# Kernel optimization log

Measured on AMD Instinct MI355X. Metric: run time of the kernel, lower is better.

## Reference

```python
import jax, jax.numpy as jnp
import numpy as np

LATENT, HID = 32, 64
NODE_FEAT, EDGE_FEAT, ENERGY_DIM, STRESS_DIM = 4, 3, 2, 9
B, N, E = 256, 200000, 1500000


def _lin(key, fan_in, fan_out):
    kw, kb = jax.random.split(key)
    s = 1.0 / np.sqrt(fan_in)
    return (jax.random.uniform(kw, (fan_in, fan_out), jnp.float32, -s, s),
            jax.random.uniform(kb, (fan_out,), jnp.float32, -s, s))


def setup_inputs() -> dict:
    key = jax.random.key(0)
    ks = jax.random.split(key, 16)
    z = jax.random.normal(ks[0], (B, LATENT), jnp.float32)
    node_emb = jax.random.normal(ks[1], (N, 2 * HID), jnp.float32)
    graph_id = jnp.sort(jax.random.randint(ks[2], (N,), 0, B))
    src = jax.random.randint(ks[3], (E,), 0, N)
    dst = jax.random.randint(ks[4], (E,), 0, N)
    lp_w, lp_b = _lin(ks[5], LATENT, 2 * HID)            # latent_proj
    nep_w, nep_b = _lin(ks[6], 2 * HID, 2 * HID)          # node_emb_proj
    nd1_w, nd1_b = _lin(ks[7], 2 * HID, HID)              # node_decoder L1
    nd2_w, nd2_b = _lin(ks[8], HID, NODE_FEAT)            # node_decoder L2
    ed1_w, ed1_b = _lin(ks[9], 4 * HID, HID)              # edge_decoder L1
    ed2_w, ed2_b = _lin(ks[10], HID, EDGE_FEAT)           # edge_decoder L2
    en1_w, en1_b = _lin(ks[11], LATENT, HID)              # energy L1
    en2_w, en2_b = _lin(ks[12], HID, ENERGY_DIM)          # energy L2
    st1_w, st1_b = _lin(ks[13], LATENT, HID)              # stress L1
    st2_w, st2_b = _lin(ks[14], HID, STRESS_DIM)          # stress L2
    return dict(z=z, node_emb=node_emb, graph_id=graph_id, src=src, dst=dst,
                lp_w=lp_w, lp_b=lp_b, nep_w=nep_w, nep_b=nep_b,
                nd1_w=nd1_w, nd1_b=nd1_b, nd2_w=nd2_w, nd2_b=nd2_b,
                ed1_w=ed1_w, ed1_b=ed1_b, ed2_w=ed2_w, ed2_b=ed2_b,
                en1_w=en1_w, en1_b=en1_b, en2_w=en2_w, en2_b=en2_b,
                st1_w=st1_w, st1_b=st1_b, st2_w=st2_w, st2_b=st2_b)


def reference(z, node_emb, graph_id, src, dst,
              lp_w, lp_b, nep_w, nep_b, nd1_w, nd1_b, nd2_w, nd2_b,
              ed1_w, ed1_b, ed2_w, ed2_b, en1_w, en1_b, en2_w, en2_b,
              st1_w, st1_b, st2_w, st2_b):
    # latent_proj + per-graph broadcast (gather replaces the Python loop)
    z_proj = jax.nn.relu(z @ lp_w + lp_b)            # [B, 2H]
    z_expanded = z_proj[graph_id]                    # [N, 2H]
    # node reconstruction (dropout is identity in eval)
    nep = jax.nn.relu(node_emb @ nep_w + nep_b)      # [N, 2H]
    h = z_expanded + nep
    recon_node = jax.nn.relu(h @ nd1_w + nd1_b) @ nd2_w + nd2_b    # [N, 4]
    # edge reconstruction: gather-concat + small MLP
    edge_input = jnp.concatenate([z_expanded[src], z_expanded[dst]], axis=1)  # [E, 4H]
    recon_edge = jax.nn.relu(edge_input @ ed1_w + ed1_b) @ ed2_w + ed2_b       # [E, 3]
    # graph-level predictors
    pred_energy = jax.nn.relu(z @ en1_w + en1_b) @ en2_w + en2_b   # [B, 2]
    pred_stress = jax.nn.relu(z @ st1_w + st1_b) @ st2_w + st2_b   # [B, 9]
    return recon_node, recon_edge, pred_energy, pred_stress
```

## Files before the change

### kernel.cpp

```cpp
#include <hip/hip_runtime.h>
#include <hip/hip_bf16.h>

#define LATENT 32
#define HID 64
#define NB 256
#define NN 200000
#define NE 1500000
#define TWOH 128

#define OUT_NODE_OFF   0
#define OUT_EDGE_OFF   (NN * 4)
#define OUT_ENERGY_OFF (OUT_EDGE_OFF + NE * 3)
#define OUT_STRESS_OFF (OUT_ENERGY_OFF + NB * 2)

#define WS_ZPROJ 0
#define WS_ZC    (WS_ZPROJ + NB*TWOH)
#define WS_P1    (WS_ZC + NB*HID)
#define WS_P2    (WS_P1 + NB*HID)
#define WS_T4    (WS_P2 + NB*HID)
#define WS_W1T   (WS_T4 + NB*NB*4)
#define WS_W2T   (WS_W1T + 8192)

typedef _Float16 half8 __attribute__((ext_vector_type(8)));
typedef _Float16 half4 __attribute__((ext_vector_type(4)));
typedef float f32x4 __attribute__((ext_vector_type(4)));

__global__ void precompute_kernel(
    const float* __restrict__ z,
    const float* __restrict__ lp_w, const float* __restrict__ lp_b,
    const float* __restrict__ nd1_w,
    const float* __restrict__ ed1_w,
    const float* __restrict__ en1_w, const float* __restrict__ en1_b,
    const float* __restrict__ en2_w, const float* __restrict__ en2_b,
    const float* __restrict__ st1_w, const float* __restrict__ st1_b,
    const float* __restrict__ st2_w, const float* __restrict__ st2_b,
    float* __restrict__ z_proj, float* __restrict__ zc,
    float* __restrict__ P1, float* __restrict__ P2,
    float* __restrict__ out_energy, float* __restrict__ out_stress)
{
    const int b = blockIdx.x;
    const int t = threadIdx.x;

    __shared__ float zrow[LATENT];
    __shared__ float zp[TWOH];
    __shared__ float h_en[HID];
    __shared__ float h_st[HID];

    if (t < LATENT) zrow[t] = z[b * LATENT + t];
    __syncthreads();

    {
        float a = lp_b[t];
        #pragma unroll
        for (int k = 0; k < LATENT; ++k)
            a = fmaf(zrow[k], lp_w[k * TWOH + t], a);
        a = fmaxf(a, 0.f);
        zp[t] = a;
        z_proj[b * TWOH + t] = a;
    }

    if (t < HID) {
        float ae = en1_b[t];
        float as = st1_b[t];
        #pragma unroll
        for (int k = 0; k < LATENT; ++k) {
            ae = fmaf(zrow[k], en1_w[k * HID + t], ae);
            as = fmaf(zrow[k], st1_w[k * HID + t], as);
        }
        h_en[t] = fmaxf(ae, 0.f);
        h_st[t] = fmaxf(as, 0.f);
    }
    __syncthreads();

    if (t < HID) {
        float a = 0.f, p1 = 0.f, p2 = 0.f;
        #pragma unroll 8
        for (int k = 0; k < TWOH; ++k) {
            const float zk = zp[k];
            a  = fmaf(zk, nd1_w[k * HID + t], a);
            p1 = fmaf(zk, ed1_w[k * HID + t], p1);
            p2 = fmaf(zk, ed1_w[(TWOH + k) * HID + t], p2);
        }
        zc[b * HID + t] = a;
        P1[b * HID + t] = p1;
        P2[b * HID + t] = p2;
    }

    if (t < 2) {
        float a = en2_b[t];
        #pragma unroll 8
        for (int k = 0; k < HID; ++k) a = fmaf(h_en[k], en2_w[k * 2 + t], a);
        out_energy[b * 2 + t] = a;
    }
    if (t >= 16 && t < 25) {
        const int j = t - 16;
        float a = st2_b[j];
        #pragma unroll 8
        for (int k = 0; k < HID; ++k) a = fmaf(h_st[k], st2_w[k * 9 + j], a);
        out_stress[b * 9 + j] = a;
    }
}

__global__ void prep_weights_kernel(
    const float* __restrict__ nep_w, const float* __restrict__ nd1_w,
    _Float16* __restrict__ w1T, _Float16* __restrict__ w2T)
{
    const int i = blockIdx.x * 256 + threadIdx.x;
    if (i < TWOH * TWOH) {
        const int n = i >> 7, k = i & 127;
        w1T[i] = (_Float16)nep_w[k * TWOH + n];
    }
    if (i < HID * TWOH) {
        const int n = i >> 7, k = i & 127;
        w2T[i] = (_Float16)nd1_w[k * HID + n];
    }
}

__global__ void edge_table_kernel(
    const float* __restrict__ P1, const float* __restrict__ P2,
    const float* __restrict__ ed1_b,
    const float* __restrict__ ed2_w, const float* __restrict__ ed2_b,
    float4* __restrict__ T4)
{
    const int gs = blockIdx.x;
    const int t  = threadIdx.x;

    __shared__ float p1s[HID];
    __shared__ float b1s[HID];
    __shared__ float w2s[HID * 3];
    __shared__ float b2s[3];

    if (t < HID) { p1s[t] = P1[gs * HID + t]; b1s[t] = ed1_b[t]; }
    if (t >= 64 && t < 64 + HID * 3) w2s[t - 64] = ed2_w[t - 64];
    if (t < 3) b2s[t] = ed2_b[t];
    __syncthreads();

    float o0 = b2s[0], o1 = b2s[1], o2 = b2s[2];
    const float* __restrict__ p2 = &P2[t * HID];
    #pragma unroll 8
    for (int k = 0; k < HID; ++k) {
        float h = fmaxf(p1s[k] + p2[k] + b1s[k], 0.f);
        o0 = fmaf(h, w2s[k * 3 + 0], o0);
        o1 = fmaf(h, w2s[k * 3 + 1], o1);
        o2 = fmaf(h, w2s[k * 3 + 2], o2);
    }
    T4[gs * NB + t] = make_float4(o0, o1, o2, 0.f);
}

#define MT 64
#define SWZ(r) (((r) & 15) << 3)

__global__ __launch_bounds__(256, 2)
void node_kernel(
    const float* __restrict__ node_emb,
    const int*   __restrict__ graph_id,
    const _Float16* __restrict__ w1T,
    const float* __restrict__ nep_b,
    const _Float16* __restrict__ w2T,
    const float* __restrict__ nd1_b,
    const float* __restrict__ nd2_w, const float* __restrict__ nd2_b,
    const float* __restrict__ zc,
    float* __restrict__ out_node)
{
    __shared__ _Float16 embT[MT * TWOH];
    __shared__ _Float16 nep [MT * TWOH];
    __shared__ float    tt  [MT * 69];
    __shared__ float    w3  [HID * 4];
    __shared__ int      gid_s[MT];

    const int tid = threadIdx.x;
    const int n0  = blockIdx.x * MT;

    {
        const int c4 = tid & 31;
        #pragma unroll
        for (int pass = 0; pass < 8; ++pass) {
            const int row = (tid >> 5) + pass * 8;
            const float4 v = *reinterpret_cast<const float4*>(
                node_emb + (size_t)(n0 + row) * TWOH + c4 * 4);
            half4 h;
            h[0] = (_Float16)v.x; h[1] = (_Float16)v.y;
            h[2] = (_Float16)v.z; h[3] = (_Float16)v.w;
            const int e = row * TWOH + c4 * 4;
            *reinterpret_cast<half4*>(&embT[e ^ SWZ(row)]) = h;
        }
        if (tid < MT) gid_s[tid] = graph_id[n0 + tid];
        w3[tid] = nd2_w[tid];
    }
    __syncthreads();

    const int wv   = tid >> 6;
    const int lane = tid & 63;
    const int lrow = lane & 15;
    const int kg   = lane >> 4;

    {
        half8 a[4];
        #pragma unroll
        for (int kb = 0; kb < 4; ++kb) {
            const int r = wv * 16 + lrow;
            const int e = r * TWOH + kb * 32 + kg * 8;
            a[kb] = *reinterpret_cast<const half8*>(&embT[e ^ SWZ(r)]);
        }
        f32x4 acc[8];
        #pragma unroll
        for (int tn = 0; tn < 8; ++tn) acc[tn] = (f32x4){0.f, 0.f, 0.f, 0.f};

        #pragma unroll
        for (int tn = 0; tn < 8; ++tn) {
            const int n = tn * 16 + lrow;
            #pragma unroll
            for (int kb = 0; kb < 4; ++kb) {
                const half8 b = *reinterpret_cast<const half8*>(
                    &w1T[n * TWOH + kb * 32 + kg * 8]);
                acc[tn] = __builtin_amdgcn_mfma_f32_16x16x32_f16(a[kb], b, acc[tn], 0, 0, 0);
            }
        }
        #pragma unroll
        for (int tn = 0; tn < 8; ++tn) {
            const int n = tn * 16 + lrow;
            const float bn = nep_b[n];
            #pragma unroll
            for (int reg = 0; reg < 4; ++reg) {
                const int r = wv * 16 + kg * 4 + reg;
                const float v = fmaxf(acc[tn][reg] + bn, 0.f);
                nep[(r * TWOH + n) ^ SWZ(r)] = (_Float16)v;
            }
        }
    }
    __syncthreads();

    {
        half8 a2[4];
        #pragma unroll
        for (int kb = 0; kb < 4; ++kb) {
            const int r = wv * 16 + lrow;
            const int e = r * TWOH + kb * 32 + kg * 8;
            a2[kb] = *reinterpret_cast<const half8*>(&nep[e ^ SWZ(r)]);
        }
        f32x4 acc2[4];
        #pragma unroll
        for (int tn = 0; tn < 4; ++tn) acc2[tn] = (f32x4){0.f, 0.f, 0.f, 0.f};

        #pragma unroll
        for (int tn = 0; tn < 4; ++tn) {
            const int n = tn * 16 + lrow;
            #pragma unroll
            for (int kb = 0; kb < 4; ++kb) {
                const half8 b = *reinterpret_cast<const half8*>(
                    &w2T[n * TWOH + kb * 32 + kg * 8]);
                acc2[tn] = __builtin_amdgcn_mfma_f32_16x16x32_f16(a2[kb], b, acc2[tn], 0, 0, 0);
            }
        }
        #pragma unroll
        for (int tn = 0; tn < 4; ++tn) {
            const int n = tn * 16 + lrow;
            const float b1 = nd1_b[n];
            #pragma unroll
            for (int reg = 0; reg < 4; ++reg) {
                const int r = wv * 16 + kg * 4 + reg;
                const int g = gid_s[r];
                const float v = fmaxf(acc2[tn][reg] + b1 + zc[g * HID + n], 0.f);
                tt[r * 69 + n] = v;
            }
        }
    }
    __syncthreads();

    {
        const int nd = tid >> 2;
        const int o  = tid & 3;
        float a = nd2_b[o];
        #pragma unroll 8
        for (int k = 0; k < HID; ++k)
            a = fmaf(tt[nd * 69 + k], w3[k * 4 + o], a);
        out_node[(size_t)(n0 + nd) * 4 + o] = a;
    }
}

__global__ void edge_kernel(
    const int* __restrict__ src, const int* __restrict__ dst,
    const int* __restrict__ graph_id,
    const float4* __restrict__ T4,
    float* __restrict__ out_edge)
{
    const int e0 = (blockIdx.x * 256 + threadIdx.x) * 4;
    if (e0 >= NE) return;
    const int4 s4 = *reinterpret_cast<const int4*>(&src[e0]);
    const int4 d4 = *reinterpret_cast<const int4*>(&dst[e0]);
    const int ss[4] = {s4.x, s4.y, s4.z, s4.w};
    const int dd[4] = {d4.x, d4.y, d4.z, d4.w};
    float o[12];
    #pragma unroll
    for (int j = 0; j < 4; ++j) {
        const int gs = graph_id[ss[j]];
        const int gd = graph_id[dd[j]];
        const float4 t = T4[gs * NB + gd];
        o[j * 3 + 0] = t.x; o[j * 3 + 1] = t.y; o[j * 3 + 2] = t.z;
    }
    float4* outp = reinterpret_cast<float4*>(&out_edge[(size_t)e0 * 3]);
    outp[0] = make_float4(o[0], o[1], o[2],  o[3]);
    outp[1] = make_float4(o[4], o[5], o[6],  o[7]);
    outp[2] = make_float4(o[8], o[9], o[10], o[11]);
}

extern "C" void kernel_launch(void* const* d_in, const int* in_sizes, int n_in,
                              void* d_out, int out_size, void* d_ws, size_t ws_size,
                              hipStream_t stream)
{
    const float* z        = (const float*)d_in[0];
    const float* node_emb = (const float*)d_in[1];
    const int*   graph_id = (const int*)  d_in[2];
    const int*   src      = (const int*)  d_in[3];
    const int*   dst      = (const int*)  d_in[4];
    const float* lp_w  = (const float*)d_in[5];
    const float* lp_b  = (const float*)d_in[6];
    const float* nep_w = (const float*)d_in[7];
    const float* nep_b = (const float*)d_in[8];
    const float* nd1_w = (const float*)d_in[9];
    const float* nd1_b = (const float*)d_in[10];
    const float* nd2_w = (const float*)d_in[11];
    const float* nd2_b = (const float*)d_in[12];
    const float* ed1_w = (const float*)d_in[13];
    const float* ed1_b = (const float*)d_in[14];
    const float* ed2_w = (const float*)d_in[15];
    const float* ed2_b = (const float*)d_in[16];
    const float* en1_w = (const float*)d_in[17];
    const float* en1_b = (const float*)d_in[18];
    const float* en2_w = (const float*)d_in[19];
    const float* en2_b = (const float*)d_in[20];
    const float* st1_w = (const float*)d_in[21];
    const float* st1_b = (const float*)d_in[22];
    const float* st2_w = (const float*)d_in[23];
    const float* st2_b = (const float*)d_in[24];

    float* out = (float*)d_out;
    float* out_node   = out + OUT_NODE_OFF;
    float* out_edge   = out + OUT_EDGE_OFF;
    float* out_energy = out + OUT_ENERGY_OFF;
    float* out_stress = out + OUT_STRESS_OFF;

    float* ws     = (float*)d_ws;
    float* z_proj = ws + WS_ZPROJ;
    float* zc     = ws + WS_ZC;
    float* P1     = ws + WS_P1;
    float* P2     = ws + WS_P2;
    float4* T4    = (float4*)(ws + WS_T4);
    _Float16* w1T = (_Float16*)(ws + WS_W1T);
    _Float16* w2T = (_Float16*)(ws + WS_W2T);

    precompute_kernel<<<NB, 128, 0, stream>>>(
        z, lp_w, lp_b, nd1_w, ed1_w,
        en1_w, en1_b, en2_w, en2_b, st1_w, st1_b, st2_w, st2_b,
        z_proj, zc, P1, P2, out_energy, out_stress);

    prep_weights_kernel<<<64, 256, 0, stream>>>(nep_w, nd1_w, w1T, w2T);

    edge_table_kernel<<<NB, NB, 0, stream>>>(P1, P2, ed1_b, ed2_w, ed2_b, T4);

    node_kernel<<<NN / MT, 256, 0, stream>>>(
        node_emb, graph_id, w1T, nep_b, w2T, nd1_b, nd2_w, nd2_b,
        zc, out_node);

    edge_kernel<<<(NE / 4 + 255) / 256, 256, 0, stream>>>(
        src, dst, graph_id, T4, out_edge);
}
```

Before: 310.6 us.

## Fuse node and edge kernels into persistent pipelined kernel with register-resident weights

Merges the node MLP and edge gather kernels into one launch. Node blocks become persistent (512 blocks looping over tiles) and double-buffer the node_emb tile, prefetching the next tile into registers while MFMAs run on the current one. Weights are held in registers as the A operand instead of being reloaded from global memory for every tile. The final layer becomes a register dot product plus cross-lane shuffle reduction instead of a shared-memory loop. Weight prep is also folded into the precompute launch to save a kernel launch. The cost is higher register pressure and fewer node blocks, which may limit occupancy or parallelism.

```diff
diff --git a/kernel.cpp b/kernel.cpp
--- a/kernel.cpp
+++ b/kernel.cpp
@@ -24,6 +24,12 @@
 typedef _Float16 half8 __attribute__((ext_vector_type(8)));
 typedef _Float16 half4 __attribute__((ext_vector_type(4)));
 typedef float f32x4 __attribute__((ext_vector_type(4)));
+
+#define MT 64
+#define NTILES (NN / MT)
+#define NODE_BLOCKS 512
+#define EDGE_BLOCKS ((NE / 4 + 255) / 256)
+#define SWZ(r) (((r) & 15) << 3)
 
 __global__ void precompute_kernel(
     const float* __restrict__ z,
@@ -34,13 +40,28 @@
     const float* __restrict__ en2_w, const float* __restrict__ en2_b,
     const float* __restrict__ st1_w, const float* __restrict__ st1_b,
     const float* __restrict__ st2_w, const float* __restrict__ st2_b,
+    const float* __restrict__ nep_w,
     float* __restrict__ z_proj, float* __restrict__ zc,
     float* __restrict__ P1, float* __restrict__ P2,
+    _Float16* __restrict__ w1T, _Float16* __restrict__ w2T,
     float* __restrict__ out_energy, float* __restrict__ out_stress)
 {
+    const int t = threadIdx.x;
+
+    if (blockIdx.x >= NB) {
+        const int i = (blockIdx.x - NB) * 256 + t;
+        if (i < TWOH * TWOH) {
+            const int n = i >> 7, k = i & 127;
+            w1T[i] = (_Float16)nep_w[k * TWOH + n];
+        }
+        if (i < HID * TWOH) {
+            const int n = i >> 7, k = i & 127;
+            w2T[i] = (_Float16)nd1_w[k * HID + n];
+        }
+        return;
+    }
+
     const int b = blockIdx.x;
-    const int t = threadIdx.x;
-
     __shared__ float zrow[LATENT];
     __shared__ float zp[TWOH];
     __shared__ float h_en[HID];
@@ -49,7 +70,7 @@
     if (t < LATENT) zrow[t] = z[b * LATENT + t];
     __syncthreads();
 
-    {
+    if (t < TWOH) {
         float a = lp_b[t];
         #pragma unroll
         for (int k = 0; k < LATENT; ++k)
@@ -58,7 +79,6 @@
         zp[t] = a;
         z_proj[b * TWOH + t] = a;
     }
-
     if (t < HID) {
         float ae = en1_b[t];
         float as = st1_b[t];
@@ -85,7 +105,6 @@
         P1[b * HID + t] = p1;
         P2[b * HID + t] = p2;
     }
-
     if (t < 2) {
         float a = en2_b[t];
         #pragma unroll 8
@@ -98,21 +117,6 @@
         #pragma unroll 8
         for (int k = 0; k < HID; ++k) a = fmaf(h_st[k], st2_w[k * 9 + j], a);
         out_stress[b * 9 + j] = a;
-    }
-}
-
-__global__ void prep_weights_kernel(
-    const float* __restrict__ nep_w, const float* __restrict__ nd1_w,
-    _Float16* __restrict__ w1T, _Float16* __restrict__ w2T)
-{
-    const int i = blockIdx.x * 256 + threadIdx.x;
-    if (i < TWOH * TWOH) {
-        const int n = i >> 7, k = i & 127;
-        w1T[i] = (_Float16)nep_w[k * TWOH + n];
-    }
-    if (i < HID * TWOH) {
-        const int n = i >> 7, k = i & 127;
-        w2T[i] = (_Float16)nd1_w[k * HID + n];
     }
 }
 
@@ -147,11 +151,8 @@
     T4[gs * NB + t] = make_float4(o0, o1, o2, 0.f);
 }
 
-#define MT 64
-#define SWZ(r) (((r) & 15) << 3)
-
 __global__ __launch_bounds__(256, 2)
-void node_kernel(
+void node_edge_kernel(
     const float* __restrict__ node_emb,
     const int*   __restrict__ graph_id,
     const _Float16* __restrict__ w1T,
@@ -160,148 +161,219 @@
     const float* __restrict__ nd1_b,
     const float* __restrict__ nd2_w, const float* __restrict__ nd2_b,
     const float* __restrict__ zc,
-    float* __restrict__ out_node)
+    const int* __restrict__ src, const int* __restrict__ dst,
+    const float4* __restrict__ T4,
+    float* __restrict__ out_node, float* __restrict__ out_edge)
 {
-    __shared__ _Float16 embT[MT * TWOH];
-    __shared__ _Float16 nep [MT * TWOH];
-    __shared__ float    tt  [MT * 69];
-    __shared__ float    w3  [HID * 4];
-    __shared__ int      gid_s[MT];
-
     const int tid = threadIdx.x;
-    const int n0  = blockIdx.x * MT;
-
-    {
-        const int c4 = tid & 31;
-        #pragma unroll
-        for (int pass = 0; pass < 8; ++pass) {
-            const int row = (tid >> 5) + pass * 8;
-            const float4 v = *reinterpret_cast<const float4*>(
-                node_emb + (size_t)(n0 + row) * TWOH + c4 * 4);
-            half4 h;
-            h[0] = (_Float16)v.x; h[1] = (_Float16)v.y;
-            h[2] = (_Float16)v.z; h[3] = (_Float16)v.w;
-            const int e = row * TWOH + c4 * 4;
-            *reinterpret_cast<half4*>(&embT[e ^ SWZ(row)]) = h;
-        }
-        if (tid < MT) gid_s[tid] = graph_id[n0 + tid];
-        w3[tid] = nd2_w[tid];
-    }
-    __syncthreads();
+    const int bid = blockIdx.x;
+
+    if (bid >= NODE_BLOCKS) {
+        const int e0 = ((bid - NODE_BLOCKS) * 256 + tid) * 4;
+        if (e0 >= NE) return;
+        const int4 s4 = *reinterpret_cast<const int4*>(&src[e0]);
+        const int4 d4 = *reinterpret_cast<const int4*>(&dst[e0]);
+        const int ss[4] = {s4.x, s4.y, s4.z, s4.w};
+        const int dd[4] = {d4.x, d4.y, d4.z, d4.w};
+        float o[12];
+        #pragma unroll
+        for (int j = 0; j < 4; ++j) {
+            const int gs = graph_id[ss[j]];
+            const int gd = graph_id[dd[j]];
+            const float4 tv = T4[gs * NB + gd];
+            o[j * 3 + 0] = tv.x; o[j * 3 + 1] = tv.y; o[j * 3 + 2] = tv.z;
+        }
+        float4* outp = reinterpret_cast<float4*>(&out_edge[(size_t)e0 * 3]);
+        outp[0] = make_float4(o[0], o[1], o[2],  o[3]);
+        outp[1] = make_float4(o[4], o[5], o[6],  o[7]);
+        outp[2] = make_float4(o[8], o[9], o[10], o[11]);
+        return;
+    }
+
+    __shared__ _Float16 embL[2][MT * TWOH];
+    __shared__ _Float16 nepL[MT * TWOH];
+    __shared__ float    partL[4 * MT * 4];
+    __shared__ int      gidL[2][MT];
 
     const int wv   = tid >> 6;
     const int lane = tid & 63;
     const int lrow = lane & 15;
     const int kg   = lane >> 4;
 
+    half8 w1A[2][4];
+    half8 w2A[4];
+    #pragma unroll
+    for (int cht = 0; cht < 2; ++cht)
+        #pragma unroll
+        for (int kb = 0; kb < 4; ++kb)
+            w1A[cht][kb] = *reinterpret_cast<const half8*>(
+                &w1T[(wv * 32 + cht * 16 + lrow) * TWOH + kb * 32 + kg * 8]);
+    #pragma unroll
+    for (int kb = 0; kb < 4; ++kb)
+        w2A[kb] = *reinterpret_cast<const half8*>(
+            &w2T[(wv * 16 + lrow) * TWOH + kb * 32 + kg * 8]);
+
+    f32x4 b1r[2], b2r, w3r[4];
+    #pragma unroll
+    for (int cht = 0; cht < 2; ++cht)
+        b1r[cht] = *reinterpret_cast<const f32x4*>(&nep_b[wv * 32 + cht * 16 + kg * 4]);
+    b2r = *reinterpret_cast<const f32x4*>(&nd1_b[wv * 16 + kg * 4]);
+    #pragma unroll
+    for (int j = 0; j < 4; ++j)
+        w3r[j] = *reinterpret_cast<const f32x4*>(&nd2_w[(wv * 16 + kg * 4 + j) * 4]);
+    const float b3 = nd2_b[tid & 3];
+
+    const int r0 = tid >> 2;
+    const int q0 = tid & 3;
+
     {
-        half8 a[4];
-        #pragma unroll
-        for (int kb = 0; kb < 4; ++kb) {
-            const int r = wv * 16 + lrow;
-            const int e = r * TWOH + kb * 32 + kg * 8;
-            a[kb] = *reinterpret_cast<const half8*>(&embT[e ^ SWZ(r)]);
-        }
-        f32x4 acc[8];
-        #pragma unroll
-        for (int tn = 0; tn < 8; ++tn) acc[tn] = (f32x4){0.f, 0.f, 0.f, 0.f};
-
-        #pragma unroll
-        for (int tn = 0; tn < 8; ++tn) {
-            const int n = tn * 16 + lrow;
+        const float4* s4 = reinterpret_cast<const float4*>(
+            node_emb + (size_t)(bid * MT + r0) * TWOH);
+        float4 rr[8];
+        #pragma unroll
+        for (int p = 0; p < 8; ++p) rr[p] = s4[q0 + 4 * p];
+        #pragma unroll
+        for (int p = 0; p < 8; ++p) {
+            half4 h;
+            h[0] = (_Float16)rr[p].x; h[1] = (_Float16)rr[p].y;
+            h[2] = (_Float16)rr[p].z; h[3] = (_Float16)rr[p].w;
+            const int e = r0 * TWOH + (q0 + 4 * p) * 4;
+            *reinterpret_cast<half4*>(&embL[0][e ^ SWZ(r0)]) = h;
+        }
+        if (tid < MT) gidL[0][tid] = graph_id[bid * MT + tid];
+    }
+    __syncthreads();
+
+    int cur = 0;
+    for (int t = bid; t < NTILES; t += NODE_BLOCKS) {
+        const int tn = t + NODE_BLOCKS;
+        const bool have_next = (tn < NTILES);
+
+        float4 rr[8];
+        int gnext = 0;
+        if (have_next) {
+            const float4* s4 = reinterpret_cast<const float4*>(
+                node_emb + (size_t)(tn * MT + r0) * TWOH);
+            #pragma unroll
+            for (int p = 0; p < 8; ++p) rr[p] = s4[q0 + 4 * p];
+            if (tid < MT) gnext = graph_id[tn * MT + tid];
+        }
+
+        const _Float16* eb = embL[cur];
+
+        f32x4 acc1[2][4];
+        #pragma unroll
+        for (int cht = 0; cht < 2; ++cht)
+            #pragma unroll
+            for (int nt = 0; nt < 4; ++nt)
+                acc1[cht][nt] = (f32x4){0.f, 0.f, 0.f, 0.f};
+
+        #pragma unroll
+        for (int nt = 0; nt < 4; ++nt) {
+            half8 eB[4];
             #pragma unroll
             for (int kb = 0; kb < 4; ++kb) {
-                const half8 b = *reinterpret_cast<const half8*>(
-                    &w1T[n * TWOH + kb * 32 + kg * 8]);
-                acc[tn] = __builtin_amdgcn_mfma_f32_16x16x32_f16(a[kb], b, acc[tn], 0, 0, 0);
+                const int row = nt * 16 + lrow;
+                const int e = row * TWOH + kb * 32 + kg * 8;
+                eB[kb] = *reinterpret_cast<const half8*>(&eb[e ^ SWZ(row)]);
             }
-        }
-        #pragma unroll
-        for (int tn = 0; tn < 8; ++tn) {
-            const int n = tn * 16 + lrow;
-            const float bn = nep_b[n];
-            #pragma unroll
-            for (int reg = 0; reg < 4; ++reg) {
-                const int r = wv * 16 + kg * 4 + reg;
-                const float v = fmaxf(acc[tn][reg] + bn, 0.f);
-                nep[(r * TWOH + n) ^ SWZ(r)] = (_Float16)v;
+            #pragma unroll
+            for (int cht = 0; cht < 2; ++cht)
+                #pragma unroll
+                for (int kb = 0; kb < 4; ++kb)
+                    acc1[cht][nt] = __builtin_amdgcn_mfma_f32_16x16x32_f16(
+                        w1A[cht][kb], eB[kb], acc1[cht][nt], 0, 0, 0);
+        }
+        #pragma unroll
+        for (int cht = 0; cht < 2; ++cht)
+            #pragma unroll
+            for (int nt = 0; nt < 4; ++nt) {
+                const int node = nt * 16 + lrow;
+                const int ch = wv * 32 + cht * 16 + kg * 4;
+                half4 h;
+                #pragma unroll
+                for (int j = 0; j < 4; ++j)
+                    h[j] = (_Float16)fmaxf(acc1[cht][nt][j] + b1r[cht][j], 0.f);
+                *reinterpret_cast<half4*>(
+                    &nepL[(node * TWOH + ch) ^ SWZ(node)]) = h;
             }
-        }
-    }
-    __syncthreads();
-
-    {
-        half8 a2[4];
-        #pragma unroll
-        for (int kb = 0; kb < 4; ++kb) {
-            const int r = wv * 16 + lrow;
-            const int e = r * TWOH + kb * 32 + kg * 8;
-            a2[kb] = *reinterpret_cast<const half8*>(&nep[e ^ SWZ(r)]);
-        }
+        __syncthreads();
+
         f32x4 acc2[4];
         #pragma unroll
-        for (int tn = 0; tn < 4; ++tn) acc2[tn] = (f32x4){0.f, 0.f, 0.f, 0.f};
-
-        #pragma unroll
-        for (int tn = 0; tn < 4; ++tn) {
-            const int n = tn * 16 + lrow;
+        for (int nt = 0; nt < 4; ++nt) acc2[nt] = (f32x4){0.f, 0.f, 0.f, 0.f};
+
+        #pragma unroll
+        for (int nt = 0; nt < 4; ++nt) {
+            half8 nB[4];
             #pragma unroll
             for (int kb = 0; kb < 4; ++kb) {
-                const half8 b = *reinterpret_cast<const half8*>(
-                    &w2T[n * TWOH + kb * 32 + kg * 8]);
-                acc2[tn] = __builtin_amdgcn_mfma_f32_16x16x32_f16(a2[kb], b, acc2[tn], 0, 0, 0);
+                const int row = nt * 16 + lrow;
+                const int e = row * TWOH + kb * 32 + kg * 8;
+                nB[kb] = *reinterpret_cast<const half8*>(&nepL[e ^ SWZ(row)]);
             }
-        }
-        #pragma unroll
-        for (int tn = 0; tn < 4; ++tn) {
-            const int n = tn * 16 + lrow;
-            const float b1 = nd1_b[n];
-            #pragma unroll
-            for (int reg = 0; reg < 4; ++reg) {
-                const int r = wv * 16 + kg * 4 + reg;
-                const int g = gid_s[r];
-                const float v = fmaxf(acc2[tn][reg] + b1 + zc[g * HID + n], 0.f);
-                tt[r * 69 + n] = v;
+            #pragma unroll
+            for (int kb = 0; kb < 4; ++kb)
+                acc2[nt] = __builtin_amdgcn_mfma_f32_16x16x32_f16(
+                    w2A[kb], nB[kb], acc2[nt], 0, 0, 0);
+        }
+
+        f32x4 p[4];
+        #pragma unroll
+        for (int nt = 0; nt < 4; ++nt) {
+            const int node = nt * 16 + lrow;
+            const int g = gidL[cur][node];
+            const f32x4 z4 = *reinterpret_cast<const f32x4*>(
+                &zc[(size_t)g * HID + wv * 16 + kg * 4]);
+            f32x4 t4;
+            #pragma unroll
+            for (int j = 0; j < 4; ++j)
+                t4[j] = fmaxf(acc2[nt][j] + b2r[j] + z4[j], 0.f);
+            f32x4 pp = t4[0] * w3r[0];
+            pp += t4[1] * w3r[1];
+            pp += t4[2] * w3r[2];
+            pp += t4[3] * w3r[3];
+            p[nt] = pp;
+        }
+        #pragma unroll
+        for (int nt = 0; nt < 4; ++nt) {
+            #pragma unroll
+            for (int j = 0; j < 4; ++j) {
+                p[nt][j] += __shfl_xor(p[nt][j], 16, 64);
+                p[nt][j] += __shfl_xor(p[nt][j], 32, 64);
             }
         }
-    }
-    __syncthreads();
-
-    {
-        const int nd = tid >> 2;
-        const int o  = tid & 3;
-        float a = nd2_b[o];
-        #pragma unroll 8
-        for (int k = 0; k < HID; ++k)
-            a = fmaf(tt[nd * 69 + k], w3[k * 4 + o], a);
-        out_node[(size_t)(n0 + nd) * 4 + o] = a;
-    }
-}
-
-__global__ void edge_kernel(
-    const int* __restrict__ src, const int* __restrict__ dst,
-    const int* __restrict__ graph_id,
-    const float4* __restrict__ T4,
-    float* __restrict__ out_edge)
-{
-    const int e0 = (blockIdx.x * 256 + threadIdx.x) * 4;
-    if (e0 >= NE) return;
-    const int4 s4 = *reinterpret_cast<const int4*>(&src[e0]);
-    const int4 d4 = *reinterpret_cast<const int4*>(&dst[e0]);
-    const int ss[4] = {s4.x, s4.y, s4.z, s4.w};
-    const int dd[4] = {d4.x, d4.y, d4.z, d4.w};
-    float o[12];
-    #pragma unroll
-    for (int j = 0; j < 4; ++j) {
-        const int gs = graph_id[ss[j]];
-        const int gd = graph_id[dd[j]];
-        const float4 t = T4[gs * NB + gd];
-        o[j * 3 + 0] = t.x; o[j * 3 + 1] = t.y; o[j * 3 + 2] = t.z;
-    }
-    float4* outp = reinterpret_cast<float4*>(&out_edge[(size_t)e0 * 3]);
-    outp[0] = make_float4(o[0], o[1], o[2],  o[3]);
-    outp[1] = make_float4(o[4], o[5], o[6],  o[7]);
-    outp[2] = make_float4(o[8], o[9], o[10], o[11]);
+        if (lane < 16) {
+            #pragma unroll
+            for (int nt = 0; nt < 4; ++nt)
+                *reinterpret_cast<f32x4*>(
+                    &partL[(wv * MT + nt * 16 + lrow) * 4]) = p[nt];
+        }
+        __syncthreads();
+
+        {
+            const int node = r0;
+            const int o    = q0;
+            const int ix = node * 4 + o;
+            const float s = partL[ix] + partL[256 + ix] +
+                            partL[512 + ix] + partL[768 + ix] + b3;
+            out_node[(size_t)(t * MT + node) * 4 + o] = s;
+        }
+
+        if (have_next) {
+            #pragma unroll
+            for (int p8 = 0; p8 < 8; ++p8) {
+                half4 h;
+                h[0] = (_Float16)rr[p8].x; h[1] = (_Float16)rr[p8].y;
+                h[2] = (_Float16)rr[p8].z; h[3] = (_Float16)rr[p8].w;
+                const int e = r0 * TWOH + (q0 + 4 * p8) * 4;
+                *reinterpret_cast<half4*>(&embL[cur ^ 1][e ^ SWZ(r0)]) = h;
+            }
+            if (tid < MT) gidL[cur ^ 1][tid] = gnext;
+        }
+        __syncthreads();
+        cur ^= 1;
+    }
 }
 
 extern "C" void kernel_launch(void* const* d_in, const int* in_sizes, int n_in,
@@ -349,19 +421,14 @@
     _Float16* w1T = (_Float16*)(ws + WS_W1T);
     _Float16* w2T = (_Float16*)(ws + WS_W2T);
 
-    precompute_kernel<<<NB, 128, 0, stream>>>(
+    precompute_kernel<<<NB + 64, 256, 0, stream>>>(
         z, lp_w, lp_b, nd1_w, ed1_w,
-        en1_w, en1_b, en2_w, en2_b, st1_w, st1_b, st2_w, st2_b,
-        z_proj, zc, P1, P2, out_energy, out_stress);
-
-    prep_weights_kernel<<<64, 256, 0, stream>>>(nep_w, nd1_w, w1T, w2T);
+        en1_w, en1_b, en2_w, en2_b, st1_w, st1_b, st2_w, st2_b, nep_w,
+        z_proj, zc, P1, P2, w1T, w2T, out_energy, out_stress);
 
     edge_table_kernel<<<NB, NB, 0, stream>>>(P1, P2, ed1_b, ed2_w, ed2_b, T4);
 
-    node_kernel<<<NN / MT, 256, 0, stream>>>(
-        node_emb, graph_id, w1T, nep_b, w2T, nd1_b, nd2_w, nd2_b,
-        zc, out_node);
-
-    edge_kernel<<<(NE / 4 + 255) / 256, 256, 0, stream>>>(
-        src, dst, graph_id, T4, out_edge);
+    node_edge_kernel<<<NODE_BLOCKS + EDGE_BLOCKS, 256, 0, stream>>>(
+        node_emb, graph_id, w1T, nep_b, w2T, nd1_b, nd2_w, nd2_b, zc,
+        src, dst, T4, out_node, out_edge);
 }
```

Measured after the change: 249.5 us. 1.24x faster.
